# Kernel tuning notes

Measured on AMD Instinct MI355X. Metric: run time of the kernel, lower is better.

The kernel has to match this reference:

```python
import jax, jax.numpy as jnp
import numpy as np
import math

D_MODEL = 1024
N_HEADS = 16
D_HEAD = 64
D_MLP = 4096
N_LAYERS = 12
INIT_STD = 0.02
EPS = 1e-5
BATCH = 2
SEQ = 2048


def setup_inputs() -> dict:
    key = jax.random.key(0)
    ks = jax.random.split(key, 8)
    attn_std = INIT_STD
    proj_std = INIT_STD / math.sqrt(2 * N_LAYERS)
    return {
        "resid_pre": jax.random.normal(ks[0], (BATCH, SEQ, D_MODEL), jnp.float32),
        "ln1_w": jnp.ones((D_MODEL,), jnp.float32),
        "ln1_b": jnp.zeros((D_MODEL,), jnp.float32),
        "W_Q": attn_std * jax.random.normal(ks[1], (N_HEADS, D_MODEL, D_HEAD), jnp.float32),
        "b_Q": jnp.zeros((N_HEADS, D_HEAD), jnp.float32),
        "W_K": attn_std * jax.random.normal(ks[2], (N_HEADS, D_MODEL, D_HEAD), jnp.float32),
        "b_K": jnp.zeros((N_HEADS, D_HEAD), jnp.float32),
        "W_V": attn_std * jax.random.normal(ks[3], (N_HEADS, D_MODEL, D_HEAD), jnp.float32),
        "b_V": jnp.zeros((N_HEADS, D_HEAD), jnp.float32),
        "W_O": proj_std * jax.random.normal(ks[4], (N_HEADS, D_HEAD, D_MODEL), jnp.float32),
        "b_O": jnp.zeros((D_MODEL,), jnp.float32),
        "ln2_w": jnp.ones((D_MODEL,), jnp.float32),
        "ln2_b": jnp.zeros((D_MODEL,), jnp.float32),
        "W_in": INIT_STD * jax.random.normal(ks[5], (D_MODEL, D_MLP), jnp.float32),
        "b_in": jnp.zeros((D_MLP,), jnp.float32),
        "W_out": proj_std * jax.random.normal(ks[6], (D_MLP, D_MODEL), jnp.float32),
        "b_out": jnp.zeros((D_MODEL,), jnp.float32),
    }


def _layernorm(x, w, b):
    mean = x.mean(-1, keepdims=True)
    var = x.var(-1, keepdims=True)  # unbiased=False
    return (x - mean) / jnp.sqrt(var + EPS) * w + b


def _attention(x, W_Q, b_Q, W_K, b_K, W_V, b_V, W_O, b_O):
    # x: [b, s, d]; W_*: [h, d, k]
    q = jnp.einsum('bsd,hdk->bshk', x, W_Q) + b_Q
    k = jnp.einsum('bsd,hdk->bshk', x, W_K) + b_K
    v = jnp.einsum('bsd,hdk->bshk', x, W_V) + b_V
    scores = jnp.einsum('bqhk,bshk->bhqs', q, k) / math.sqrt(D_HEAD)
    seq = x.shape[1]
    causal = jnp.tril(jnp.ones((seq, seq), bool))
    scores = jnp.where(causal, scores, -jnp.inf)
    pattern = jax.nn.softmax(scores, axis=-1)
    z = jnp.einsum('bhqs,bshk->bqhk', pattern, v)
    return jnp.einsum('bqhk,hkd->bqd', z, W_O) + b_O


def reference(resid_pre, ln1_w, ln1_b, W_Q, b_Q, W_K, b_K, W_V, b_V, W_O, b_O,
              ln2_w, ln2_b, W_in, b_in, W_out, b_out):
    attn_out = _attention(_layernorm(resid_pre, ln1_w, ln1_b),
                          W_Q, b_Q, W_K, b_K, W_V, b_V, W_O, b_O)
    resid_mid = resid_pre + attn_out
    h = _layernorm(resid_mid, ln2_w, ln2_b)
    mlp_out = jnp.matmul(jax.nn.relu(jnp.matmul(h, W_in) + b_in), W_out) + b_out
    return resid_mid + mlp_out
```

## Files before the change

### kernel.cpp

```cpp
#include <hip/hip_runtime.h>
#include <stdint.h>


typedef unsigned short u16;
typedef __bf16 bf16x8 __attribute__((ext_vector_type(8)));
typedef __bf16 bf16x4 __attribute__((ext_vector_type(4)));
typedef __bf16 bf16x2 __attribute__((ext_vector_type(2)));
typedef short  s16x4  __attribute__((ext_vector_type(4)));
typedef float  f32x4  __attribute__((ext_vector_type(4)));

#define QSCALE 0.18033688011112042f

__device__ __forceinline__ float bf2f(unsigned int u) {
  union { unsigned int u; float f; } v; v.u = u << 16; return v.f;
}
__device__ __forceinline__ u16 f2bf(float f) {
  union { float f; unsigned int u; } v; v.f = f;
  unsigned int r = v.u + 0x7FFFu + ((v.u >> 16) & 1u);
  return (u16)(r >> 16);
}
__device__ __forceinline__ unsigned pkbf(float lo, float hi) {
#if __has_builtin(__builtin_amdgcn_cvt_pk_bf16_f32)
  bf16x2 t = __builtin_amdgcn_cvt_pk_bf16_f32(lo, hi);
  return __builtin_bit_cast(unsigned, t);
#else
  return (unsigned)f2bf(lo) | ((unsigned)f2bf(hi) << 16);
#endif
}
__device__ __forceinline__ float loadf(const void* p, size_t i, int isf) {
  return isf ? ((const float*)p)[i] : bf2f(((const u16*)p)[i]);
}

__device__ __forceinline__ f32x4 mfma16(s16x4 a, s16x4 b, f32x4 c) {
#if __has_builtin(__builtin_amdgcn_mfma_f32_16x16x16_bf16)
  return __builtin_amdgcn_mfma_f32_16x16x16_bf16(
      __builtin_bit_cast(bf16x4, a), __builtin_bit_cast(bf16x4, b), c, 0, 0, 0);
#else
  return __builtin_amdgcn_mfma_f32_16x16x16bf16_1k(a, b, c, 0, 0, 0);
#endif
}

__global__ __launch_bounds__(256) void detect_dtype(
    const unsigned int* __restrict__ x, int* __restrict__ flag) {
  __shared__ int cnt;
  if (threadIdx.x == 0) cnt = 0;
  __syncthreads();
  int c = 0;
  for (int i = threadIdx.x; i < 512; i += 256) {
    unsigned int e = (x[i] >> 23) & 0xFFu;
    if (e >= 97u && e <= 157u) c++;
  }
  atomicAdd(&cnt, c);
  __syncthreads();
  if (threadIdx.x == 0) *flag = (cnt > 384) ? 1 : 0;
}

__global__ __launch_bounds__(256) void pack_qkv_tiled(
    const int* __restrict__ flagp,
    const void* __restrict__ Wq, const void* __restrict__ Wk, const void* __restrict__ Wv,
    u16* __restrict__ WT) {
  __shared__ float t[64][65];
  const int isf = *flagp;
  const int tid = threadIdx.x;
  const int mh = blockIdx.y;
  const int mat = mh >> 4, h = mh & 15;
  const int d0 = blockIdx.x << 6;
  const void* src = (mat == 0) ? Wq : (mat == 1) ? Wk : Wv;
  const float scale = (mat == 0) ? QSCALE : 1.f;
  const int lane = tid & 63, rr = tid >> 6;
  const size_t sbase = ((size_t)h << 16) + lane;
#pragma unroll
  for (int i = 0; i < 16; i++) {
    int d = i * 4 + rr;
    t[d][lane] = loadf(src, sbase + (size_t)(d0 + d) * 64, isf) * scale;
  }
  __syncthreads();
#pragma unroll
  for (int i = 0; i < 16; i++) {
    int k = i * 4 + rr;
    WT[((size_t)((mat << 10) + (h << 6) + k) << 10) + d0 + lane] = f2bf(t[lane][k]);
  }
}

__global__ __launch_bounds__(256) void transpose_tiled(
    const int* __restrict__ flagp, const void* __restrict__ src,
    u16* __restrict__ dst, int R, int C) {
  __shared__ float t[64][65];
  const int isf = *flagp;
  const int tid = threadIdx.x;
  const int c0 = blockIdx.x << 6, r0 = blockIdx.y << 6;
  const int lane = tid & 63, rr = tid >> 6;
#pragma unroll
  for (int i = 0; i < 16; i++) {
    int r = i * 4 + rr;
    t[r][lane] = loadf(src, (size_t)(r0 + r) * C + c0 + lane, isf);
  }
  __syncthreads();
#pragma unroll
  for (int i = 0; i < 16; i++) {
    int c = i * 4 + rr;
    dst[(size_t)(c0 + c) * R + r0 + lane] = f2bf(t[lane][c]);
  }
}

__global__ __launch_bounds__(256) void pack_biases(
    const int* __restrict__ flagp,
    const void* bq, const void* bk, const void* bv,
    const void* bO, const void* bin, const void* bout,
    float* __restrict__ out) {
  const int isf = *flagp;
  int i = blockIdx.x * 256 + threadIdx.x;
  float v;
  if (i < 1024)      v = loadf(bq,   i,        isf) * QSCALE;
  else if (i < 2048) v = loadf(bk,   i - 1024, isf);
  else if (i < 3072) v = loadf(bv,   i - 2048, isf);
  else if (i < 4096) v = loadf(bO,   i - 3072, isf);
  else if (i < 8192) v = loadf(bin,  i - 4096, isf);
  else               v = loadf(bout, i - 8192, isf);
  out[i] = v;
}

template<int SRC>
__global__ __launch_bounds__(256) void ln_fwd(
    const int* __restrict__ flagp, const void* __restrict__ xin,
    const void* __restrict__ w, const void* __restrict__ b,
    u16* __restrict__ out) {
  const int isf = *flagp;
  const int row = blockIdx.x, tid = threadIdx.x;
  const int col = tid << 2;
  const size_t base = ((size_t)row << 10) + col;
  float v[4];
#pragma unroll
  for (int i = 0; i < 4; i++)
    v[i] = (SRC == 1) ? ((const float*)xin)[base + i] : loadf(xin, base + i, isf);
  float s  = v[0] + v[1] + v[2] + v[3];
  float ss = v[0]*v[0] + v[1]*v[1] + v[2]*v[2] + v[3]*v[3];
#pragma unroll
  for (int mk = 32; mk >= 1; mk >>= 1) {
    s  += __shfl_xor(s,  mk, 64);
    ss += __shfl_xor(ss, mk, 64);
  }
  __shared__ float red[8];
  if ((tid & 63) == 0) { red[tid >> 6] = s; red[4 + (tid >> 6)] = ss; }
  __syncthreads();
  float S  = red[0] + red[1] + red[2] + red[3];
  float SS = red[4] + red[5] + red[6] + red[7];
  float mean = S * (1.f / 1024.f);
  float var  = SS * (1.f / 1024.f) - mean * mean;
  float rstd = rsqrtf(var + 1e-5f);
  u16 e[4];
#pragma unroll
  for (int i = 0; i < 4; i++) {
    float wv = loadf(w, col + i, isf);
    float bv = loadf(b, col + i, isf);
    e[i] = f2bf((v[i] - mean) * rstd * wv + bv);
  }
  uint2 o;
  o.x = (unsigned)e[0] | ((unsigned)e[1] << 16);
  o.y = (unsigned)e[2] | ((unsigned)e[3] << 16);
  *(uint2*)(out + base) = o;
}

template<int MODE, int TM>
__global__ __launch_bounds__(256) void gemm_bt(
    const int* __restrict__ flagp,
    const u16* __restrict__ A, const u16* __restrict__ BT,
    const float* __restrict__ bias, const void* __restrict__ resid,
    void* __restrict__ out, void* __restrict__ out2, void* __restrict__ out3,
    int M, int N, int K, int SHL) {
  constexpr int WR = TM / 32;
  __shared__ u16 as[TM * 32];
  __shared__ u16 bs[128 * 32];
  int isf = 0;
  if (MODE == 2 || MODE == 3) isf = *flagp;
  const int Lb = blockIdx.x;
  const int xcd = Lb & 7, sidx = Lb >> 3;
  const int SH = 1 << SHL;
  const int by = xcd * SH + (sidx & (SH - 1));
  const int bx = sidx >> SHL;
  const int tid = threadIdx.x;
  const int L = tid & 63, w = tid >> 6;
  const int wm = (w >> 1) * (TM >> 1), wn = (w & 1) << 6;
  const int row0 = by * TM, col0 = bx << 7;
  const int m = L & 15, quad = L >> 4;

  f32x4 zero4 = {0.f, 0.f, 0.f, 0.f};
  f32x4 acc[WR][4];
#pragma unroll
  for (int i = 0; i < WR; i++)
#pragma unroll
    for (int j = 0; j < 4; j++) acc[i][j] = zero4;

  const int tm = tid >> 2;
  const int tk = (tid & 3) << 3;
  const u16* Ag  = A  + (size_t)(row0 + tm) * K + tk;
  const u16* Ag2 = Ag + (size_t)64 * K;
  const u16* Bg  = BT + (size_t)(col0 + tm) * K + tk;
  const u16* Bg2 = Bg + (size_t)64 * K;
  u16* asl  = &as[tid * 8];
  u16* asl2 = &as[2048 + tid * 8];
  u16* bsl  = &bs[tid * 8];
  u16* bsl2 = &bs[2048 + tid * 8];

  const int aoff = (wm + m) * 32 + quad * 8;
  const int boff = (wn + m) * 32 + quad * 8;

  int4 ar0, ar1, br0, br1;
  ar0 = *(const int4*)Ag;
  if (TM == 128) ar1 = *(const int4*)Ag2;
  br0 = *(const int4*)Bg;
  br1 = *(const int4*)Bg2;

  for (int kk = 0; kk < K; kk += 32) {
    __syncthreads();
    *(int4*)asl = ar0;
    if (TM == 128) *(int4*)asl2 = ar1;
    *(int4*)bsl = br0;
    *(int4*)bsl2 = br1;
    __syncthreads();
    if (kk + 32 < K) {
      ar0 = *(const int4*)(Ag + kk + 32);
      if (TM == 128) ar1 = *(const int4*)(Ag2 + kk + 32);
      br0 = *(const int4*)(Bg + kk + 32);
      br1 = *(const int4*)(Bg2 + kk + 32);
    }
    bf16x8 af[WR], bfr[4];
#pragma unroll
    for (int i = 0; i < WR; i++) af[i]  = *(const bf16x8*)&as[aoff + i * 512];
#pragma unroll
    for (int j = 0; j < 4; j++) bfr[j] = *(const bf16x8*)&bs[boff + j * 512];
#pragma unroll
    for (int i = 0; i < WR; i++)
#pragma unroll
      for (int j = 0; j < 4; j++)
        acc[i][j] = __builtin_amdgcn_mfma_f32_16x16x32_bf16(af[i], bfr[j], acc[i][j], 0, 0, 0);
  }

#pragma unroll
  for (int j = 0; j < 4; j++) {
    const int col = col0 + wn + j * 16 + m;
    const float bval = bias[col];
    if (MODE == 4) {
      const int sel = col >> 10;
      const int hh  = (col >> 6) & 15;
      const int f   = col & 63;
#pragma unroll
      for (int i = 0; i < WR; i++) {
        const int rowb = row0 + wm + i * 16 + quad * 4;
        if (sel < 2) {
          u16* dst = (u16*)(sel ? out2 : out);
#pragma unroll
          for (int r = 0; r < 4; r++)
            dst[((((size_t)hh << 12) + rowb + r) << 6) + f] = f2bf(acc[i][j][r] + bval);
        } else {
          uint2 o;
          o.x = pkbf(acc[i][j][0] + bval, acc[i][j][1] + bval);
          o.y = pkbf(acc[i][j][2] + bval, acc[i][j][3] + bval);
          *(uint2*)&((u16*)out3)[(((size_t)hh * 64 + f) << 12) + rowb] = o;
        }
      }
    } else {
#pragma unroll
      for (int i = 0; i < WR; i++) {
        const int rowb = row0 + wm + i * 16 + quad * 4;
#pragma unroll
        for (int r = 0; r < 4; r++) {
          float vv = acc[i][j][r] + bval;
          size_t idx = (size_t)(rowb + r) * N + col;
          if (MODE == 1) {
            ((u16*)out)[idx] = f2bf(fmaxf(vv, 0.f));
          } else if (MODE == 2) {
            ((float*)out)[idx] = vv + loadf(resid, idx, isf);
          } else if (MODE == 3) {
            float o = vv + ((const float*)resid)[idx];
            if (isf) ((float*)out)[idx] = o;
            else     ((u16*)out)[idx]   = f2bf(o);
          }
        }
      }
    }
  }
}

__global__ __launch_bounds__(256, 3) void attn_part(
    const u16* __restrict__ qh, const u16* __restrict__ kh,
    const u16* __restrict__ vT, u16* __restrict__ Opart,
    float* __restrict__ stats) {
  const int combo = blockIdx.x;
  const int qt = blockIdx.y;
  const int ci = blockIdx.z;
  const int q0 = qt << 6;
  const int nc = (q0 + 64 + 511) >> 9;
  if (ci >= nc) return;
  const int k_lo = ci << 9;
  const int k_hi = min(k_lo + 512, q0 + 64);
  const int nsteps = (k_hi - k_lo + 127) >> 7;

  __shared__ u16 kS[128 * 72];
  __shared__ u16 vS[64 * 136];
  const int tid = threadIdx.x, L = tid & 63, w = tid >> 6;
  const int m = L & 15, quad = L >> 4;
  const int h = combo >> 1, b = combo & 1;
  const size_t tb = (size_t)b * 2048;
  const size_t hbase = (size_t)h * 4096;
  const int qg = q0 + w * 16 + m;

  bf16x8 qb0, qb1;
  {
    const u16* qp = qh + ((hbase + tb + (size_t)qg) << 6) + quad * 8;
    qb0 = *(const bf16x8*)qp;
    qb1 = *(const bf16x8*)(qp + 32);
  }

  f32x4 zero4 = {0.f, 0.f, 0.f, 0.f};
  f32x4 O[4];
#pragma unroll
  for (int ft = 0; ft < 4; ft++) O[ft] = zero4;
  float mrow = -30000.f, lrow = 0.f;

  const int krow[4] = { (0*256+tid) >> 3, (1*256+tid) >> 3, (2*256+tid) >> 3, (3*256+tid) >> 3 };
  const int kc = tid & 7;
  const int vf[4] = { (0*256+tid) >> 4, (1*256+tid) >> 4, (2*256+tid) >> 4, (3*256+tid) >> 4 };
  const int vc = tid & 15;
  const int vq = (vc & 1) << 1;
  const int vk4 = (vc >> 1) << 2;
  const int vc0 = (vq << 5) + vk4;
  const int vc1 = ((vq + 1) << 5) + vk4;

  int4 kr[4], vr[4];
#pragma unroll
  for (int i = 0; i < 4; i++) {
    kr[i] = *(const int4*)(kh + ((hbase + tb + k_lo + krow[i]) << 6) + kc * 8);
    vr[i] = *(const int4*)(vT + (((size_t)h * 64 + vf[i]) << 12) + tb + k_lo + vc * 8);
  }

  for (int j = 0; j < nsteps; j++) {
    const int k0 = k_lo + (j << 7);
    __syncthreads();
#pragma unroll
    for (int i = 0; i < 4; i++) {
      *(int4*)&kS[krow[i] * 72 + kc * 8] = kr[i];
      union { int4 v; s16x4 hh[2]; } tv; tv.v = vr[i];
      *(s16x4*)&vS[vf[i] * 136 + vc0] = tv.hh[0];
      *(s16x4*)&vS[vf[i] * 136 + vc1] = tv.hh[1];
    }
    __syncthreads();
    if (j + 1 < nsteps) {
      const int k1 = k_lo + ((j + 1) << 7);
#pragma unroll
      for (int i = 0; i < 4; i++) {
        kr[i] = *(const int4*)(kh + ((hbase + tb + k1 + krow[i]) << 6) + kc * 8);
        vr[i] = *(const int4*)(vT + (((size_t)h * 64 + vf[i]) << 12) + tb + k1 + vc * 8);
      }
    }
    f32x4 sc[8];
#pragma unroll
    for (int kt = 0; kt < 8; kt++) {
      const u16* kp = &kS[(kt * 16 + m) * 72 + quad * 8];
      bf16x8 ka0 = *(const bf16x8*)kp;
      bf16x8 ka1 = *(const bf16x8*)(kp + 32);
      f32x4 t = zero4;
      t = __builtin_amdgcn_mfma_f32_16x16x32_bf16(ka0, qb0, t, 0, 0, 0);
      t = __builtin_amdgcn_mfma_f32_16x16x32_bf16(ka1, qb1, t, 0, 0, 0);
      sc[kt] = t;
    }
    if (k0 + 128 > q0) {
#pragma unroll
      for (int kt = 0; kt < 8; kt++)
#pragma unroll
        for (int r = 0; r < 4; r++) {
          int ktok = k0 + kt * 16 + quad * 4 + r;
          if (ktok > qg) sc[kt][r] = -30000.f;
        }
    }
    float mx = sc[0][0];
#pragma unroll
    for (int kt = 0; kt < 8; kt++)
#pragma unroll
      for (int r = 0; r < 4; r++) mx = fmaxf(mx, sc[kt][r]);
    mx = fmaxf(mx, __shfl_xor(mx, 16, 64));
    mx = fmaxf(mx, __shfl_xor(mx, 32, 64));
    float mnew = fmaxf(mrow, mx);
    float alpha = __builtin_amdgcn_exp2f(mrow - mnew);
    mrow = mnew;
    s16x4 pb[8];
    float sum = 0.f;
#pragma unroll
    for (int kt = 0; kt < 8; kt++) {
      float e0 = __builtin_amdgcn_exp2f(sc[kt][0] - mnew);
      float e1 = __builtin_amdgcn_exp2f(sc[kt][1] - mnew);
      float e2 = __builtin_amdgcn_exp2f(sc[kt][2] - mnew);
      float e3 = __builtin_amdgcn_exp2f(sc[kt][3] - mnew);
      sum += (e0 + e1) + (e2 + e3);
      union { uint2 u; s16x4 hh; } pu;
      pu.u.x = pkbf(e0, e1);
      pu.u.y = pkbf(e2, e3);
      pb[kt] = pu.hh;
    }
    sum += __shfl_xor(sum, 16, 64);
    sum += __shfl_xor(sum, 32, 64);
    lrow = lrow * alpha + sum;
#pragma unroll
    for (int ft = 0; ft < 4; ft++) O[ft] *= alpha;
#pragma unroll
    for (int ft = 0; ft < 4; ft++) {
      const u16* vp = &vS[(ft * 16 + m) * 136 + quad * 32];
#pragma unroll
      for (int pr = 0; pr < 4; pr++) {
        union { bf16x8 v; s16x4 hh[2]; } u;
        u.v = *(const bf16x8*)(vp + pr * 8);
        O[ft] = mfma16(u.hh[0], pb[2 * pr],     O[ft]);
        O[ft] = mfma16(u.hh[1], pb[2 * pr + 1], O[ft]);
      }
    }
  }

  __syncthreads();
#pragma unroll
  for (int ft = 0; ft < 4; ft++) {
    union { uint2 u; s16x4 hh; } o4;
    o4.u.x = pkbf(O[ft][0], O[ft][1]);
    o4.u.y = pkbf(O[ft][2], O[ft][3]);
    *(s16x4*)&kS[(w * 16 + m) * 72 + ft * 16 + quad * 4] = o4.hh;
  }
  __syncthreads();
  const int slot = (combo * 32 + qt) * 4 + ci;
  u16* op = Opart + ((size_t)slot << 12);
#pragma unroll
  for (int it = 0; it < 2; it++) {
    int idx = it * 256 + tid;
    int row = idx >> 3, c = idx & 7;
    *(int4*)&op[row * 64 + c * 8] = *(const int4*)&kS[row * 72 + c * 8];
  }
  if (quad == 0) {
    stats[slot * 128 + w * 16 + m]      = mrow;
    stats[slot * 128 + 64 + w * 16 + m] = lrow;
  }
}

__global__ __launch_bounds__(256) void attn_merge(
    const u16* __restrict__ Opart, const float* __restrict__ stats,
    u16* __restrict__ z) {
  const int combo = blockIdx.x, qt = blockIdx.y;
  const int h = combo >> 1, b = combo & 1;
  const int q0 = qt << 6;
  const int nc = (q0 + 64 + 511) >> 9;
  const int tid = threadIdx.x;
  const int t = tid >> 2, f0 = (tid & 3) << 4;
  const int slot0 = (combo * 32 + qt) * 4;
  float M = -3e4f;
  for (int ci = 0; ci < nc; ci++)
    M = fmaxf(M, stats[(slot0 + ci) * 128 + t]);
  float acc[16];
#pragma unroll
  for (int e = 0; e < 16; e++) acc[e] = 0.f;
  float ltot = 0.f;
  for (int ci = 0; ci < nc; ci++) {
    float mi = stats[(slot0 + ci) * 128 + t];
    float li = stats[(slot0 + ci) * 128 + 64 + t];
    float wgt = exp2f(mi - M);
    ltot += wgt * li;
    const u16* op = Opart + (((size_t)(slot0 + ci)) << 12) + t * 64 + f0;
    union { int4 v; u16 u[8]; } a0, a1;
    a0.v = *(const int4*)op;
    a1.v = *(const int4*)(op + 8);
#pragma unroll
    for (int e = 0; e < 8; e++) {
      acc[e]     += wgt * bf2f(a0.u[e]);
      acc[8 + e] += wgt * bf2f(a1.u[e]);
    }
  }
  float inv = 1.f / ltot;
  union { int4 v; u16 u[8]; } o0, o1;
#pragma unroll
  for (int e = 0; e < 8; e++) {
    o0.u[e] = f2bf(acc[e] * inv);
    o1.u[e] = f2bf(acc[8 + e] * inv);
  }
  size_t tok = (size_t)b * 2048 + q0 + t;
  *(int4*)&z[tok * 1024 + h * 64 + f0]     = o0.v;
  *(int4*)&z[tok * 1024 + h * 64 + f0 + 8] = o1.v;
}

extern "C" void kernel_launch(void* const* d_in, const int* in_sizes, int n_in,
                              void* d_out, int out_size, void* d_ws, size_t ws_size,
                              hipStream_t stream) {
  (void)in_sizes; (void)n_in; (void)out_size; (void)ws_size;
  const void* resid_pre = d_in[0];
  const void* ln1_w = d_in[1];
  const void* ln1_b = d_in[2];
  const void* W_Q   = d_in[3];
  const void* b_Q   = d_in[4];
  const void* W_K   = d_in[5];
  const void* b_K   = d_in[6];
  const void* W_V   = d_in[7];
  const void* b_V   = d_in[8];
  const void* W_O   = d_in[9];
  const void* b_O   = d_in[10];
  const void* ln2_w = d_in[11];
  const void* ln2_b = d_in[12];
  const void* W_in  = d_in[13];
  const void* b_in  = d_in[14];
  const void* W_out = d_in[15];
  const void* b_out = d_in[16];

  char* p = (char*)d_ws;
  auto alloc = [&](size_t bytes) {
    char* r = p; p += (bytes + 255) & ~(size_t)255; return (void*)r;
  };
  int*   flag      = (int*)  alloc(256);
  u16*   WqkvT     = (u16*)  alloc(3072ull * 1024 * 2);
  u16*   WoT       = (u16*)  alloc(1024ull * 1024 * 2);
  u16*   WinT      = (u16*)  alloc(4096ull * 1024 * 2);
  u16*   WoutT     = (u16*)  alloc(1024ull * 4096 * 2);
  float* biases    = (float*)alloc(9216 * 4);
  u16*   xn        = (u16*)  alloc(4096ull * 1024 * 2);
  u16*   q_hm      = (u16*)  alloc(16ull * 4096 * 64 * 2);
  u16*   k_hm      = (u16*)  alloc(16ull * 4096 * 64 * 2);
  u16*   vTws      = (u16*)  alloc(16ull * 64 * 4096 * 2);
  float* resid_mid = (float*)alloc(4096ull * 1024 * 4);
  u16*   h2        = (u16*)  alloc(4096ull * 1024 * 2);
  u16*   act       = (u16*)  alloc(4096ull * 4096 * 2);
  u16*   z = xn;
  u16*   Opart = act;
  float* stats = (float*)h2;

  detect_dtype<<<1, 256, 0, stream>>>((const unsigned int*)resid_pre, flag);

  pack_qkv_tiled<<<dim3(16, 48), 256, 0, stream>>>(flag, W_Q, W_K, W_V, WqkvT);
  transpose_tiled<<<dim3(16, 16), 256, 0, stream>>>(flag, W_O,   WoT,   1024, 1024);
  transpose_tiled<<<dim3(64, 16), 256, 0, stream>>>(flag, W_in,  WinT,  1024, 4096);
  transpose_tiled<<<dim3(16, 64), 256, 0, stream>>>(flag, W_out, WoutT, 4096, 1024);
  pack_biases<<<36, 256, 0, stream>>>(flag, b_Q, b_K, b_V, b_O, b_in, b_out, biases);

  ln_fwd<0><<<4096, 256, 0, stream>>>(flag, resid_pre, ln1_w, ln1_b, xn);
  gemm_bt<4, 128><<<768, 256, 0, stream>>>(
      flag, xn, WqkvT, biases, nullptr, q_hm, k_hm, vTws, 4096, 3072, 1024, 2);
  attn_part<<<dim3(32, 32, 4), 256, 0, stream>>>(q_hm, k_hm, vTws, Opart, stats);
  attn_merge<<<dim3(32, 32), 256, 0, stream>>>(Opart, stats, z);
  gemm_bt<2, 64><<<512, 256, 0, stream>>>(
      flag, z, WoT, biases + 3072, resid_pre, resid_mid, nullptr, nullptr, 4096, 1024, 1024, 3);
  ln_fwd<1><<<4096, 256, 0, stream>>>(flag, resid_mid, ln2_w, ln2_b, h2);
  gemm_bt<1, 128><<<1024, 256, 0, stream>>>(
      flag, h2, WinT, biases + 4096, nullptr, act, nullptr, nullptr, 4096, 4096, 1024, 2);
  gemm_bt<3, 64><<<512, 256, 0, stream>>>(
      flag, act, WoutT, biases + 8192, resid_mid, d_out, nullptr, nullptr, 4096, 1024, 4096, 3);
}
```

Before: 432.6 us.

## Replace LDS-staged GEMM with direct-from-global register-fragment MFMA GEMM

Removes the shared-memory staging and both __syncthreads per k-step from the bf16 GEMM. Each wave now loads its MFMA fragments straight from global memory into registers, double-buffered one step ahead. Output tiling also changes: 128-row tiles with 128 or 64 columns (WC) instead of the old TM-row × 128-column tiles. This cuts LDS traffic and barrier stalls, but loses cross-wave data sharing, so each wave re-reads operands from global/L2. That multiplies cache traffic and relies on L2 to absorb the duplicated loads.

```diff
diff --git a/kernel.cpp b/kernel.cpp
--- a/kernel.cpp
+++ b/kernel.cpp
@@ -161,83 +161,70 @@
   *(uint2*)(out + base) = o;
 }
 
-template<int MODE, int TM>
-__global__ __launch_bounds__(256) void gemm_bt(
+template<int MODE, int WC>
+__global__ __launch_bounds__(256) void gemm_flat(
     const int* __restrict__ flagp,
     const u16* __restrict__ A, const u16* __restrict__ BT,
     const float* __restrict__ bias, const void* __restrict__ resid,
     void* __restrict__ out, void* __restrict__ out2, void* __restrict__ out3,
-    int M, int N, int K, int SHL) {
-  constexpr int WR = TM / 32;
-  __shared__ u16 as[TM * 32];
-  __shared__ u16 bs[128 * 32];
+    int M, int N, int K) {
   int isf = 0;
   if (MODE == 2 || MODE == 3) isf = *flagp;
   const int Lb = blockIdx.x;
   const int xcd = Lb & 7, sidx = Lb >> 3;
-  const int SH = 1 << SHL;
-  const int by = xcd * SH + (sidx & (SH - 1));
-  const int bx = sidx >> SHL;
+  const int by = xcd * 4 + (sidx & 3);
+  const int bx = sidx >> 2;
   const int tid = threadIdx.x;
   const int L = tid & 63, w = tid >> 6;
-  const int wm = (w >> 1) * (TM >> 1), wn = (w & 1) << 6;
-  const int row0 = by * TM, col0 = bx << 7;
+  const int wm = (w >> 1) << 6;
+  const int wn = (w & 1) * (WC * 16);
+  const int row0 = by << 7, col0 = bx * (WC * 32);
   const int m = L & 15, quad = L >> 4;
 
   f32x4 zero4 = {0.f, 0.f, 0.f, 0.f};
-  f32x4 acc[WR][4];
-#pragma unroll
-  for (int i = 0; i < WR; i++)
-#pragma unroll
-    for (int j = 0; j < 4; j++) acc[i][j] = zero4;
-
-  const int tm = tid >> 2;
-  const int tk = (tid & 3) << 3;
-  const u16* Ag  = A  + (size_t)(row0 + tm) * K + tk;
-  const u16* Ag2 = Ag + (size_t)64 * K;
-  const u16* Bg  = BT + (size_t)(col0 + tm) * K + tk;
-  const u16* Bg2 = Bg + (size_t)64 * K;
-  u16* asl  = &as[tid * 8];
-  u16* asl2 = &as[2048 + tid * 8];
-  u16* bsl  = &bs[tid * 8];
-  u16* bsl2 = &bs[2048 + tid * 8];
-
-  const int aoff = (wm + m) * 32 + quad * 8;
-  const int boff = (wn + m) * 32 + quad * 8;
-
-  int4 ar0, ar1, br0, br1;
-  ar0 = *(const int4*)Ag;
-  if (TM == 128) ar1 = *(const int4*)Ag2;
-  br0 = *(const int4*)Bg;
-  br1 = *(const int4*)Bg2;
-
+  f32x4 acc[4][WC];
+#pragma unroll
+  for (int i = 0; i < 4; i++)
+#pragma unroll
+    for (int j = 0; j < WC; j++) acc[i][j] = zero4;
+
+  const u16* Ap[4];
+  const u16* Bp[WC];
+#pragma unroll
+  for (int i = 0; i < 4; i++)
+    Ap[i] = A + (size_t)(row0 + wm + i * 16 + m) * K + quad * 8;
+#pragma unroll
+  for (int j = 0; j < WC; j++)
+    Bp[j] = BT + (size_t)(col0 + wn + j * 16 + m) * K + quad * 8;
+
+  bf16x8 ac[4], bc[WC];
+#pragma unroll
+  for (int i = 0; i < 4; i++) ac[i] = *(const bf16x8*)Ap[i];
+#pragma unroll
+  for (int j = 0; j < WC; j++) bc[j] = *(const bf16x8*)Bp[j];
+
+#pragma unroll 4
   for (int kk = 0; kk < K; kk += 32) {
-    __syncthreads();
-    *(int4*)asl = ar0;
-    if (TM == 128) *(int4*)asl2 = ar1;
-    *(int4*)bsl = br0;
-    *(int4*)bsl2 = br1;
-    __syncthreads();
+    bf16x8 an[4], bn[WC];
     if (kk + 32 < K) {
-      ar0 = *(const int4*)(Ag + kk + 32);
-      if (TM == 128) ar1 = *(const int4*)(Ag2 + kk + 32);
-      br0 = *(const int4*)(Bg + kk + 32);
-      br1 = *(const int4*)(Bg2 + kk + 32);
-    }
-    bf16x8 af[WR], bfr[4];
-#pragma unroll
-    for (int i = 0; i < WR; i++) af[i]  = *(const bf16x8*)&as[aoff + i * 512];
-#pragma unroll
-    for (int j = 0; j < 4; j++) bfr[j] = *(const bf16x8*)&bs[boff + j * 512];
-#pragma unroll
-    for (int i = 0; i < WR; i++)
-#pragma unroll
-      for (int j = 0; j < 4; j++)
-        acc[i][j] = __builtin_amdgcn_mfma_f32_16x16x32_bf16(af[i], bfr[j], acc[i][j], 0, 0, 0);
-  }
-
-#pragma unroll
-  for (int j = 0; j < 4; j++) {
+#pragma unroll
+      for (int i = 0; i < 4; i++) an[i] = *(const bf16x8*)(Ap[i] + kk + 32);
+#pragma unroll
+      for (int j = 0; j < WC; j++) bn[j] = *(const bf16x8*)(Bp[j] + kk + 32);
+    }
+#pragma unroll
+    for (int i = 0; i < 4; i++)
+#pragma unroll
+      for (int j = 0; j < WC; j++)
+        acc[i][j] = __builtin_amdgcn_mfma_f32_16x16x32_bf16(ac[i], bc[j], acc[i][j], 0, 0, 0);
+#pragma unroll
+    for (int i = 0; i < 4; i++) ac[i] = an[i];
+#pragma unroll
+    for (int j = 0; j < WC; j++) bc[j] = bn[j];
+  }
+
+#pragma unroll
+  for (int j = 0; j < WC; j++) {
     const int col = col0 + wn + j * 16 + m;
     const float bval = bias[col];
     if (MODE == 4) {
@@ -245,7 +232,7 @@
       const int hh  = (col >> 6) & 15;
       const int f   = col & 63;
 #pragma unroll
-      for (int i = 0; i < WR; i++) {
+      for (int i = 0; i < 4; i++) {
         const int rowb = row0 + wm + i * 16 + quad * 4;
         if (sel < 2) {
           u16* dst = (u16*)(sel ? out2 : out);
@@ -261,7 +248,7 @@
       }
     } else {
 #pragma unroll
-      for (int i = 0; i < WR; i++) {
+      for (int i = 0; i < 4; i++) {
         const int rowb = row0 + wm + i * 16 + quad * 4;
 #pragma unroll
         for (int r = 0; r < 4; r++) {
@@ -534,15 +521,15 @@
   pack_biases<<<36, 256, 0, stream>>>(flag, b_Q, b_K, b_V, b_O, b_in, b_out, biases);
 
   ln_fwd<0><<<4096, 256, 0, stream>>>(flag, resid_pre, ln1_w, ln1_b, xn);
-  gemm_bt<4, 128><<<768, 256, 0, stream>>>(
-      flag, xn, WqkvT, biases, nullptr, q_hm, k_hm, vTws, 4096, 3072, 1024, 2);
+  gemm_flat<4, 4><<<768, 256, 0, stream>>>(
+      flag, xn, WqkvT, biases, nullptr, q_hm, k_hm, vTws, 4096, 3072, 1024);
   attn_part<<<dim3(32, 32, 4), 256, 0, stream>>>(q_hm, k_hm, vTws, Opart, stats);
   attn_merge<<<dim3(32, 32), 256, 0, stream>>>(Opart, stats, z);
-  gemm_bt<2, 64><<<512, 256, 0, stream>>>(
-      flag, z, WoT, biases + 3072, resid_pre, resid_mid, nullptr, nullptr, 4096, 1024, 1024, 3);
+  gemm_flat<2, 2><<<512, 256, 0, stream>>>(
+      flag, z, WoT, biases + 3072, resid_pre, resid_mid, nullptr, nullptr, 4096, 1024, 1024);
   ln_fwd<1><<<4096, 256, 0, stream>>>(flag, resid_mid, ln2_w, ln2_b, h2);
-  gemm_bt<1, 128><<<1024, 256, 0, stream>>>(
-      flag, h2, WinT, biases + 4096, nullptr, act, nullptr, nullptr, 4096, 4096, 1024, 2);
-  gemm_bt<3, 64><<<512, 256, 0, stream>>>(
-      flag, act, WoutT, biases + 8192, resid_mid, d_out, nullptr, nullptr, 4096, 1024, 4096, 3);
-}
+  gemm_flat<1, 4><<<1024, 256, 0, stream>>>(
+      flag, h2, WinT, biases + 4096, nullptr, act, nullptr, nullptr, 4096, 4096, 1024);
+  gemm_flat<3, 2><<<512, 256, 0, stream>>>(
+      flag, act, WoutT, biases + 8192, resid_mid, d_out, nullptr, nullptr, 4096, 1024, 4096);
+}
```

After: 702.8 us. 62.5% more time.
